# Kernel optimization log

Measured on AMD Instinct MI355X. Metric: run time of the kernel, lower is better.

Reference implementation:

```python
import jax, jax.numpy as jnp
import numpy as np

B, S, D, H = 2, 2048, 2048, 8  # n_seq must equal hidden_dim (attn_net consumes the key axis)
DK = D // H
SCALING = DK ** -0.5
NEG = -1e9  # stand-in for -inf so fp16/bf16 also work


def setup_inputs() -> dict:
    key = jax.random.key(0)
    ks = jax.random.split(key, 12)
    w = lambda k, shp: (jax.random.normal(k, shp, dtype=jnp.float32) * 0.02)
    return {
        "x": jax.random.normal(ks[0], (B, S, D), dtype=jnp.float32),
        "x_mask": jax.random.randint(ks[1], (1, S), 0, 2).astype(jnp.int32),  # 1 = masked
        "Wq": w(ks[2], (D, D)), "bq": jnp.zeros((D,), jnp.float32),
        "Wk": w(ks[3], (D, D)), "bk": jnp.zeros((D,), jnp.float32),
        "Wv": w(ks[4], (D, D)), "bv": jnp.zeros((D,), jnp.float32),
        "Wa": w(ks[5], (D,)),   "ba": jnp.zeros((1,), jnp.float32),
        "Wp": w(ks[6], (D, D)), "bp": jnp.zeros((D,), jnp.float32),
    }


def reference(x, x_mask, Wq, bq, Wk, bk, Wv, bv, Wa, ba, Wp, bp):
    b, s, d = x.shape
    heads = lambda t: t.reshape(b, s, H, DK).transpose(0, 2, 1, 3)  # [B,H,S,DK]
    q = heads(x @ Wq.T + bq)
    k = heads(x @ Wk.T + bk)
    v = heads(x @ Wv.T + bv)
    # custom additive attention: QK^T -> leaky_relu -> linear score -> scale
    e = jax.nn.leaky_relu(jnp.einsum('bhid,bhjd->bhij', q, k), 0.1)   # [B,H,S,S]
    score = SCALING * (jnp.einsum('bhij,j->bhi', e, Wa) + ba[0])      # [B,H,S] one score per token
    # mask-fill (masked_fill semantics: True -> -inf) then softmax over tokens
    score = jnp.where(x_mask[:, None, :] != 0, NEG, score)
    attn = jax.nn.softmax(score, axis=-1)                             # [B,H,S]
    out = jnp.einsum('bhs,bhsd->bhd', attn, v).reshape(b, d)          # pooled [B,D]
    return jnp.tanh(out @ Wp.T + bp)                                  # [B,D]
```

## Files before the change

### kernel.cpp

```cpp
#include <hip/hip_runtime.h>
#include <hip/hip_bf16.h>
#include <stdint.h>

#define B_ 2
#define S_ 2048
#define D_ 2048
#define H_ 8
#define DK_ 256
#define SCALE_ 0.0625f
#define NEG_ -1e9f

typedef __hip_bfloat16 bf16;
typedef __attribute__((ext_vector_type(4))) float f32x4;
typedef __attribute__((ext_vector_type(8))) short bf16x8;
typedef unsigned int u32;

__device__ inline void gload_lds16(const void* g, void* l) {
  __builtin_amdgcn_global_load_lds(
      (const __attribute__((address_space(1))) u32*)g,
      (__attribute__((address_space(3))) u32*)l, 16, 0, 0);
}

__global__ void cvt_all_kernel(const float* __restrict__ x, bf16* __restrict__ xo,
                               const float* __restrict__ wq, bf16* __restrict__ wqo,
                               const float* __restrict__ wk, bf16* __restrict__ wko,
                               int nX4, int nW4) {
  int i = blockIdx.x * 256 + threadIdx.x;
  const float* in; bf16* out; int idx;
  if (i < nX4) { in = x; out = xo; idx = i; }
  else if (i < nX4 + nW4) { in = wq; out = wqo; idx = i - nX4; }
  else { in = wk; out = wko; idx = i - nX4 - nW4; }
  float4 v = ((const float4*)in)[idx];
  ushort4 o;
  o.x = __builtin_bit_cast(unsigned short, __float2bfloat16(v.x));
  o.y = __builtin_bit_cast(unsigned short, __float2bfloat16(v.y));
  o.z = __builtin_bit_cast(unsigned short, __float2bfloat16(v.z));
  o.w = __builtin_bit_cast(unsigned short, __float2bfloat16(v.w));
  ((ushort4*)out)[idx] = o;
}

__global__ __launch_bounds__(256, 2) void gemm_qk(
    const bf16* __restrict__ A,
    const bf16* __restrict__ W0, const float* __restrict__ b0, bf16* __restrict__ C0,
    const bf16* __restrict__ W1, const float* __restrict__ b1, bf16* __restrict__ C1) {
  const int Kd = D_;
  const bf16* Bm = blockIdx.z ? W1 : W0;
  const float* bias = blockIdx.z ? b1 : b0;
  bf16* C = blockIdx.z ? C1 : C0;

  __shared__ bf16 As[128 * 64];
  __shared__ bf16 Bs[128 * 64];
  const int tid = threadIdx.x;
  const int lane = tid & 63;
  const int w = tid >> 6;
  const int wr = w >> 1, wc = w & 1;
  const int bm = blockIdx.y, bn = blockIdx.x;

  f32x4 acc[4][4] = {};
  const int l8r = lane >> 3;
  const int l8c = (lane & 7) * 8;

  for (int kt = 0; kt < Kd; kt += 64) {
#pragma unroll
    for (int cc = 0; cc < 4; ++cc) {
      int chunk = w * 4 + cc;
      int rowa = bm * 128 + chunk * 8 + l8r;
      gload_lds16(A + (size_t)rowa * Kd + kt + l8c, (char*)As + chunk * 1024);
      int rowb = bn * 128 + chunk * 8 + l8r;
      gload_lds16(Bm + (size_t)rowb * Kd + kt + l8c, (char*)Bs + chunk * 1024);
    }
    __syncthreads();
#pragma unroll
    for (int kk = 0; kk < 2; ++kk) {
      const int kloc = kk * 32 + (lane >> 4) * 8;
      bf16x8 af[4], bfr[4];
#pragma unroll
      for (int mi = 0; mi < 4; ++mi) {
        int row = wr * 64 + mi * 16 + (lane & 15);
        af[mi] = *(const bf16x8*)&As[row * 64 + kloc];
      }
#pragma unroll
      for (int ni = 0; ni < 4; ++ni) {
        int row = wc * 64 + ni * 16 + (lane & 15);
        bfr[ni] = *(const bf16x8*)&Bs[row * 64 + kloc];
      }
#pragma unroll
      for (int mi = 0; mi < 4; ++mi)
#pragma unroll
        for (int ni = 0; ni < 4; ++ni)
          acc[mi][ni] = __builtin_amdgcn_mfma_f32_16x16x32_bf16(af[mi], bfr[ni], acc[mi][ni], 0, 0, 0);
    }
    __syncthreads();
  }
#pragma unroll
  for (int ni = 0; ni < 4; ++ni) {
    int col = bn * 128 + wc * 64 + ni * 16 + (lane & 15);
    int h = col >> 8, dk = col & 255;
    float bb = bias[col];
#pragma unroll
    for (int mi = 0; mi < 4; ++mi) {
      int rbase = bm * 128 + wr * 64 + mi * 16 + (lane >> 4) * 4;
#pragma unroll
      for (int r = 0; r < 4; ++r) {
        int row = rbase + r;
        int b = row >> 11, s = row & 2047;
        C[(((size_t)b * H_ + h) * S_ + s) * DK_ + dk] = __float2bfloat16(acc[mi][ni][r] + bb);
      }
    }
  }
}

__global__ __launch_bounds__(256, 2) void score_kernel(
    const bf16* __restrict__ Qh, const bf16* __restrict__ Kh,
    const float* __restrict__ Wa, float* __restrict__ score) {
  __shared__ bf16 Qs[128 * 64];
  __shared__ bf16 Ks[128 * 64];
  __shared__ float sred[2][128];
  const int tid = threadIdx.x;
  const int lane = tid & 63;
  const int w = tid >> 6;
  const int wr = w >> 1, wc = w & 1;
  const int bh = blockIdx.x, bm = blockIdx.y, bn = blockIdx.z;

  const bf16* Qbase = Qh + (size_t)bh * S_ * DK_;
  const bf16* Kbase = Kh + (size_t)bh * S_ * DK_;

  f32x4 acc[4][4] = {};
  const int l8r = lane >> 3;
  const int l8c = (lane & 7) * 8;

  for (int kt = 0; kt < DK_; kt += 64) {
#pragma unroll
    for (int cc = 0; cc < 4; ++cc) {
      int chunk = w * 4 + cc;
      int rowa = bm * 128 + chunk * 8 + l8r;
      gload_lds16(Qbase + (size_t)rowa * DK_ + kt + l8c, (char*)Qs + chunk * 1024);
      int rowb = bn * 128 + chunk * 8 + l8r;
      gload_lds16(Kbase + (size_t)rowb * DK_ + kt + l8c, (char*)Ks + chunk * 1024);
    }
    __syncthreads();
#pragma unroll
    for (int kk = 0; kk < 2; ++kk) {
      const int kloc = kk * 32 + (lane >> 4) * 8;
      bf16x8 af[4], bfr[4];
#pragma unroll
      for (int mi = 0; mi < 4; ++mi) {
        int row = wr * 64 + mi * 16 + (lane & 15);
        af[mi] = *(const bf16x8*)&Qs[row * 64 + kloc];
      }
#pragma unroll
      for (int ni = 0; ni < 4; ++ni) {
        int row = wc * 64 + ni * 16 + (lane & 15);
        bfr[ni] = *(const bf16x8*)&Ks[row * 64 + kloc];
      }
#pragma unroll
      for (int mi = 0; mi < 4; ++mi)
#pragma unroll
        for (int ni = 0; ni < 4; ++ni)
          acc[mi][ni] = __builtin_amdgcn_mfma_f32_16x16x32_bf16(af[mi], bfr[ni], acc[mi][ni], 0, 0, 0);
    }
    __syncthreads();
  }
  float wa_v[4];
#pragma unroll
  for (int ni = 0; ni < 4; ++ni)
    wa_v[ni] = Wa[bn * 128 + wc * 64 + ni * 16 + (lane & 15)];
  float psum[4][4] = {};
#pragma unroll
  for (int mi = 0; mi < 4; ++mi)
#pragma unroll
    for (int ni = 0; ni < 4; ++ni)
#pragma unroll
      for (int r = 0; r < 4; ++r) {
        float v = acc[mi][ni][r];
        v = (v > 0.f) ? v : 0.1f * v;
        psum[mi][r] += v * wa_v[ni];
      }
#pragma unroll
  for (int mi = 0; mi < 4; ++mi)
#pragma unroll
    for (int r = 0; r < 4; ++r) {
      float v = psum[mi][r];
      v += __shfl_xor(v, 1); v += __shfl_xor(v, 2);
      v += __shfl_xor(v, 4); v += __shfl_xor(v, 8);
      if ((lane & 15) == 0) {
        int lrow = wr * 64 + mi * 16 + ((lane >> 4) * 4) + r;
        sred[wc][lrow] = v;
      }
    }
  __syncthreads();
  if (tid < 128)
    atomicAdd(&score[(size_t)bh * S_ + bm * 128 + tid], sred[0][tid] + sred[1][tid]);
}

__global__ __launch_bounds__(256) void softmax_kernel(
    const float* __restrict__ score, const int* __restrict__ xmask,
    const float* __restrict__ ba, float* __restrict__ attn) {
  const int bh = blockIdx.x, tid = threadIdx.x;
  const int lane = tid & 63, w = tid >> 6;
  __shared__ float redm[4], reds[4];
  const float ba0 = ba[0];
  float loc[8];
  float mx = -3.4e38f;
#pragma unroll
  for (int t = 0; t < 8; ++t) {
    int i = t * 256 + tid;
    float s = SCALE_ * (score[(size_t)bh * S_ + i] + ba0);
    if (xmask[i] != 0) s = NEG_;
    loc[t] = s;
    mx = fmaxf(mx, s);
  }
  for (int m = 1; m < 64; m <<= 1) mx = fmaxf(mx, __shfl_xor(mx, m));
  if (lane == 0) redm[w] = mx;
  __syncthreads();
  mx = fmaxf(fmaxf(redm[0], redm[1]), fmaxf(redm[2], redm[3]));
  float sum = 0.f;
#pragma unroll
  for (int t = 0; t < 8; ++t) {
    loc[t] = expf(loc[t] - mx);
    sum += loc[t];
  }
  for (int m = 1; m < 64; m <<= 1) sum += __shfl_xor(sum, m);
  if (lane == 0) reds[w] = sum;
  __syncthreads();
  sum = reds[0] + reds[1] + reds[2] + reds[3];
  const float inv = 1.f / sum;
#pragma unroll
  for (int t = 0; t < 8; ++t) attn[(size_t)bh * S_ + t * 256 + tid] = loc[t] * inv;
}

__global__ __launch_bounds__(256) void xbar_part_kernel(
    const float* __restrict__ x, const float* __restrict__ attn, float* __restrict__ part) {
  const int cblk = blockIdx.x, sblk = blockIdx.y, b = blockIdx.z;
  const int tid = threadIdx.x;
  const int c = cblk * 1024 + tid * 4;
  __shared__ float at_s[8][32];
  for (int i = tid; i < 8 * 32; i += 256) {
    int h = i >> 5, s = i & 31;
    at_s[h][s] = attn[((size_t)b * H_ + h) * S_ + sblk * 32 + s];
  }
  __syncthreads();
  float acc[8][4] = {};
  const float* xp = x + ((size_t)b * S_ + sblk * 32) * D_ + c;
#pragma unroll 8
  for (int s = 0; s < 32; ++s) {
    float4 xv = *(const float4*)(xp + (size_t)s * D_);
#pragma unroll
    for (int h = 0; h < 8; ++h) {
      float a = at_s[h][s];
      acc[h][0] += a * xv.x; acc[h][1] += a * xv.y;
      acc[h][2] += a * xv.z; acc[h][3] += a * xv.w;
    }
  }
  float* pp = part + (((size_t)sblk * B_ + b) * H_) * D_ + c;
#pragma unroll
  for (int h = 0; h < 8; ++h)
    *(float4*)(pp + (size_t)h * D_) = *(const float4*)&acc[h][0];
}

__global__ __launch_bounds__(256) void xbar_reduce_kernel(
    const float* __restrict__ part, float* __restrict__ xbar) {
  const int idx = blockIdx.x * 256 + threadIdx.x;
  float s = 0.f;
#pragma unroll 8
  for (int sb = 0; sb < 64; ++sb)
    s += part[(size_t)sb * (B_ * H_ * D_) + idx];
  xbar[idx] = s;
}

__global__ __launch_bounds__(256) void pooled_kernel(
    const float* __restrict__ xbar, const float* __restrict__ Wv,
    const float* __restrict__ bv, float* __restrict__ pooled) {
  const int lane = threadIdx.x & 63;
  const int dv = blockIdx.x * 4 + (threadIdx.x >> 6);
  const int h = dv >> 8;
  const float* wrow = Wv + (size_t)dv * D_;
  const float* x0 = xbar + (size_t)h * D_;
  const float* x1 = xbar + (size_t)(H_ + h) * D_;
  float a0 = 0.f, a1 = 0.f;
  for (int c = lane; c < D_; c += 64) {
    float wv = wrow[c];
    a0 += wv * x0[c];
    a1 += wv * x1[c];
  }
  for (int m = 1; m < 64; m <<= 1) { a0 += __shfl_xor(a0, m); a1 += __shfl_xor(a1, m); }
  if (lane == 0) {
    float bb = bv[dv];
    pooled[dv] = a0 + bb;
    pooled[D_ + dv] = a1 + bb;
  }
}

__global__ __launch_bounds__(256) void final_kernel(
    const float* __restrict__ pooled, const float* __restrict__ Wp,
    const float* __restrict__ bp, float* __restrict__ out) {
  const int lane = threadIdx.x & 63;
  const int n = blockIdx.x * 4 + (threadIdx.x >> 6);
  const float* wrow = Wp + (size_t)n * D_;
  float a0 = 0.f, a1 = 0.f;
  for (int c = lane; c < D_; c += 64) {
    float wv = wrow[c];
    a0 += wv * pooled[c];
    a1 += wv * pooled[D_ + c];
  }
  for (int m = 1; m < 64; m <<= 1) { a0 += __shfl_xor(a0, m); a1 += __shfl_xor(a1, m); }
  if (lane == 0) {
    float bb = bp[n];
    out[n] = tanhf(a0 + bb);
    out[D_ + n] = tanhf(a1 + bb);
  }
}

extern "C" void kernel_launch(void* const* d_in, const int* in_sizes, int n_in,
                              void* d_out, int out_size, void* d_ws, size_t ws_size,
                              hipStream_t stream) {
  const float* x = (const float*)d_in[0];
  const int* xmask = (const int*)d_in[1];
  const float* Wq = (const float*)d_in[2];
  const float* bq = (const float*)d_in[3];
  const float* Wk = (const float*)d_in[4];
  const float* bk = (const float*)d_in[5];
  const float* Wv = (const float*)d_in[6];
  const float* bv = (const float*)d_in[7];
  const float* Wa = (const float*)d_in[8];
  const float* ba = (const float*)d_in[9];
  const float* Wp = (const float*)d_in[10];
  const float* bp = (const float*)d_in[11];
  float* out = (float*)d_out;

  char* ws = (char*)d_ws;
  bf16* Xb = (bf16*)ws;    ws += (size_t)B_ * S_ * D_ * 2;
  bf16* Wqb = (bf16*)ws;   ws += (size_t)D_ * D_ * 2;
  bf16* Wkb = (bf16*)ws;   ws += (size_t)D_ * D_ * 2;
  bf16* Qb = (bf16*)ws;    ws += (size_t)B_ * S_ * D_ * 2;
  bf16* Kbf = (bf16*)ws;   ws += (size_t)B_ * S_ * D_ * 2;
  float* score = (float*)ws;  ws += (size_t)B_ * H_ * S_ * 4;
  float* attn = (float*)ws;   ws += (size_t)B_ * H_ * S_ * 4;
  float* xbar = (float*)ws;   ws += (size_t)B_ * H_ * D_ * 4;
  float* pooled = (float*)ws; ws += (size_t)B_ * D_ * 4;
  float* part = (float*)Wqb;

  const int nX4 = B_ * S_ * D_ / 4, nW4 = D_ * D_ / 4;
  cvt_all_kernel<<<(nX4 + 2 * nW4) / 256, 256, 0, stream>>>(
      x, Xb, Wq, Wqb, Wk, Wkb, nX4, nW4);

  gemm_qk<<<dim3(D_ / 128, B_ * S_ / 128, 2), 256, 0, stream>>>(
      Xb, Wqb, bq, Qb, Wkb, bk, Kbf);

  hipMemsetAsync(score, 0, (size_t)B_ * H_ * S_ * 4, stream);
  score_kernel<<<dim3(B_ * H_, S_ / 128, S_ / 128), 256, 0, stream>>>(
      Qb, Kbf, Wa, score);

  softmax_kernel<<<B_ * H_, 256, 0, stream>>>(score, xmask, ba, attn);

  xbar_part_kernel<<<dim3(2, 64, B_), 256, 0, stream>>>(x, attn, part);
  xbar_reduce_kernel<<<B_ * H_ * D_ / 256, 256, 0, stream>>>(part, xbar);

  pooled_kernel<<<D_ / 4, 256, 0, stream>>>(xbar, Wv, bv, pooled);
  final_kernel<<<D_ / 4, 256, 0, stream>>>(pooled, Wp, bp, out);
}
```

Before: 343.3 us.

## Rewrite QK projection GEMM with 256x256 tiles, double-buffered LDS and swizzle

The Q/K projection GEMM moves from 128x128 tiles with 256 threads to 256x256 tiles with 512 threads. Global-to-LDS loads are double-buffered so the next K-slice loads while MFMAs run on the current one. An XOR swizzle on LDS columns avoids bank conflicts, and s_setprio is raised around MFMA bursts. The cost is 128KB of LDS per block and fewer blocks (256 total), which lowers occupancy and may leave CUs under-filled.

```diff
diff --git a/kernel.cpp b/kernel.cpp
--- a/kernel.cpp
+++ b/kernel.cpp
@@ -39,67 +39,124 @@
   ((ushort4*)out)[idx] = o;
 }
 
-__global__ __launch_bounds__(256, 2) void gemm_qk(
+__global__ __launch_bounds__(512, 2) void gemm_qk(
     const bf16* __restrict__ A,
     const bf16* __restrict__ W0, const float* __restrict__ b0, bf16* __restrict__ C0,
     const bf16* __restrict__ W1, const float* __restrict__ b1, bf16* __restrict__ C1) {
-  const int Kd = D_;
+  const int K = D_;
   const bf16* Bm = blockIdx.z ? W1 : W0;
   const float* bias = blockIdx.z ? b1 : b0;
   bf16* C = blockIdx.z ? C1 : C0;
 
-  __shared__ bf16 As[128 * 64];
-  __shared__ bf16 Bs[128 * 64];
+  __shared__ bf16 As[2][256 * 64];
+  __shared__ bf16 Bs[2][256 * 64];
   const int tid = threadIdx.x;
   const int lane = tid & 63;
   const int w = tid >> 6;
-  const int wr = w >> 1, wc = w & 1;
-  const int bm = blockIdx.y, bn = blockIdx.x;
-
-  f32x4 acc[4][4] = {};
-  const int l8r = lane >> 3;
-  const int l8c = (lane & 7) * 8;
-
-  for (int kt = 0; kt < Kd; kt += 64) {
-#pragma unroll
-    for (int cc = 0; cc < 4; ++cc) {
-      int chunk = w * 4 + cc;
-      int rowa = bm * 128 + chunk * 8 + l8r;
-      gload_lds16(A + (size_t)rowa * Kd + kt + l8c, (char*)As + chunk * 1024);
-      int rowb = bn * 128 + chunk * 8 + l8r;
-      gload_lds16(Bm + (size_t)rowb * Kd + kt + l8c, (char*)Bs + chunk * 1024);
-    }
-    __syncthreads();
-#pragma unroll
-    for (int kk = 0; kk < 2; ++kk) {
-      const int kloc = kk * 32 + (lane >> 4) * 8;
-      bf16x8 af[4], bfr[4];
-#pragma unroll
-      for (int mi = 0; mi < 4; ++mi) {
-        int row = wr * 64 + mi * 16 + (lane & 15);
-        af[mi] = *(const bf16x8*)&As[row * 64 + kloc];
-      }
-#pragma unroll
-      for (int ni = 0; ni < 4; ++ni) {
-        int row = wc * 64 + ni * 16 + (lane & 15);
-        bfr[ni] = *(const bf16x8*)&Bs[row * 64 + kloc];
-      }
-#pragma unroll
-      for (int mi = 0; mi < 4; ++mi)
-#pragma unroll
-        for (int ni = 0; ni < 4; ++ni)
-          acc[mi][ni] = __builtin_amdgcn_mfma_f32_16x16x32_bf16(af[mi], bfr[ni], acc[mi][ni], 0, 0, 0);
-    }
-    __syncthreads();
-  }
+  const int wr = w >> 2, wc = w & 3;
+  const int bn = blockIdx.x, bm = blockIdx.y;
+
+  f32x4 acc[8][4] = {};
+
+  const int srow = tid >> 3;
+  const int scol8 = ((tid & 7) ^ (srow & 7)) * 8;
+  const bf16* aSrc = A + (size_t)(bm * 256 + srow) * K + scol8;
+  const bf16* bSrc = Bm + (size_t)(bn * 256 + srow) * K + scol8;
+  char* aDst = (char*)&As[0][0] + tid * 16;
+  char* bDst = (char*)&Bs[0][0] + tid * 16;
+
+  auto STAGE = [&](int buf, int t) {
+    const int kt = t * 64;
+#pragma unroll
+    for (int c = 0; c < 4; ++c) {
+      gload_lds16(aSrc + (size_t)(c * 64) * K + kt, aDst + buf * 32768 + c * 8192);
+      gload_lds16(bSrc + (size_t)(c * 64) * K + kt, bDst + buf * 32768 + c * 8192);
+    }
+  };
+
+  const int fr = lane & 15, fk = lane >> 4;
+  const int swz = (fr & 7) << 4;
+  const char* asB = (const char*)&As[0][0];
+  const char* bsB = (const char*)&Bs[0][0];
+  const int aRow = (wr * 128 + fr) * 128;
+  const int bRow = (wc * 64 + fr) * 128;
+
+  auto READ_A = [&](int buf, int kk, bf16x8* af) {
+    const int kb = ((((kk * 4) + fk) << 4) ^ swz) + buf * 32768;
+#pragma unroll
+    for (int mi = 0; mi < 8; ++mi)
+      af[mi] = *(const bf16x8*)(asB + aRow + mi * 2048 + kb);
+  };
+  auto READ_B = [&](int buf, int kk, bf16x8* bv) {
+    const int kb = ((((kk * 4) + fk) << 4) ^ swz) + buf * 32768;
+#pragma unroll
+    for (int ni = 0; ni < 4; ++ni)
+      bv[ni] = *(const bf16x8*)(bsB + bRow + ni * 2048 + kb);
+  };
+  auto MFMA32 = [&](const bf16x8* af, const bf16x8* bv) {
+    __builtin_amdgcn_s_setprio(1);
+#pragma unroll
+    for (int mi = 0; mi < 8; ++mi)
+#pragma unroll
+      for (int ni = 0; ni < 4; ++ni)
+        acc[mi][ni] = __builtin_amdgcn_mfma_f32_16x16x32_bf16(af[mi], bv[ni], acc[mi][ni], 0, 0, 0);
+    __builtin_amdgcn_s_setprio(0);
+  };
+
+  STAGE(0, 0);
+  STAGE(1, 1);
+  asm volatile("s_waitcnt vmcnt(8)" ::: "memory");
+  __builtin_amdgcn_s_barrier();
+
+  const int NT = K / 64;
+  for (int t = 0; t < NT - 2; ++t) {
+    const int cur = t & 1;
+    {
+      bf16x8 af[8], bv[4];
+      READ_A(cur, 0, af); READ_B(cur, 0, bv);
+      MFMA32(af, bv);
+    }
+    {
+      bf16x8 af[8], bv[4];
+      READ_A(cur, 1, af); READ_B(cur, 1, bv);
+      asm volatile("s_waitcnt lgkmcnt(0)" ::: "memory");
+      __builtin_amdgcn_sched_barrier(0);
+      __builtin_amdgcn_s_barrier();
+      STAGE(cur, t + 2);
+      MFMA32(af, bv);
+      asm volatile("s_waitcnt vmcnt(8)" ::: "memory");
+      __builtin_amdgcn_s_barrier();
+    }
+  }
+  {
+    const int cur = (NT - 2) & 1;
+    bf16x8 af[8], bv[4];
+    READ_A(cur, 0, af); READ_B(cur, 0, bv);
+    MFMA32(af, bv);
+    READ_A(cur, 1, af); READ_B(cur, 1, bv);
+    asm volatile("s_waitcnt lgkmcnt(0)" ::: "memory");
+    __builtin_amdgcn_sched_barrier(0);
+    MFMA32(af, bv);
+    asm volatile("s_waitcnt vmcnt(0)" ::: "memory");
+    __builtin_amdgcn_s_barrier();
+  }
+  {
+    const int cur = (NT - 1) & 1;
+    bf16x8 af[8], bv[4];
+    READ_A(cur, 0, af); READ_B(cur, 0, bv);
+    MFMA32(af, bv);
+    READ_A(cur, 1, af); READ_B(cur, 1, bv);
+    MFMA32(af, bv);
+  }
+
 #pragma unroll
   for (int ni = 0; ni < 4; ++ni) {
-    int col = bn * 128 + wc * 64 + ni * 16 + (lane & 15);
+    int col = bn * 256 + wc * 64 + ni * 16 + (lane & 15);
     int h = col >> 8, dk = col & 255;
     float bb = bias[col];
 #pragma unroll
-    for (int mi = 0; mi < 4; ++mi) {
-      int rbase = bm * 128 + wr * 64 + mi * 16 + (lane >> 4) * 4;
+    for (int mi = 0; mi < 8; ++mi) {
+      int rbase = bm * 256 + wr * 128 + mi * 16 + (lane >> 4) * 4;
 #pragma unroll
       for (int r = 0; r < 4; ++r) {
         int row = rbase + r;
@@ -344,7 +401,7 @@
   cvt_all_kernel<<<(nX4 + 2 * nW4) / 256, 256, 0, stream>>>(
       x, Xb, Wq, Wqb, Wk, Wkb, nX4, nW4);
 
-  gemm_qk<<<dim3(D_ / 128, B_ * S_ / 128, 2), 256, 0, stream>>>(
+  gemm_qk<<<dim3(D_ / 256, B_ * S_ / 256, 2), 512, 0, stream>>>(
       Xb, Wqb, bq, Qb, Wkb, bk, Kbf);
 
   hipMemsetAsync(score, 0, (size_t)B_ * H_ * S_ * 4, stream);
```

New measurement: 311.2 us. 9.3% less time.
